# Kernel optimization log

Hardware: AMD Instinct MI355X
Metric: run time of the kernel (lower is better)

Reference implementation:

```python
import jax, jax.numpy as jnp
import numpy as np

D_MODEL = 1024
NUM_HEADS = 16
HEAD_DIM = D_MODEL // NUM_HEADS
ROT_DIM = 32
THETA = 10000.0
XPOS_SCALE_BASE = 512.0
GN_EPS = 1e-5


def setup_inputs() -> dict:
    key = jax.random.key(0)
    ks = jax.random.split(key, 12)
    d = D_MODEL
    s = 0.02
    return {
        "x": jax.random.normal(ks[0], (2, 2048, d), dtype=jnp.float32),
        "Wq": jax.random.normal(ks[1], (d, d), dtype=jnp.float32) * s,
        "bq": jnp.zeros((d,), jnp.float32),
        "Wk": jax.random.normal(ks[2], (d, d), dtype=jnp.float32) * s,
        "bk": jnp.zeros((d,), jnp.float32),
        "Wv": jax.random.normal(ks[3], (d, d), dtype=jnp.float32) * s,
        "bv": jnp.zeros((d,), jnp.float32),
        "Wg": jax.random.normal(ks[4], (d, d), dtype=jnp.float32) * s,
        "bg": jnp.zeros((d,), jnp.float32),
        "Wo": jax.random.normal(ks[5], (d, d), dtype=jnp.float32) * s,
        "bo": jnp.zeros((d,), jnp.float32),
        "gn_w": jnp.ones((NUM_HEADS,), jnp.float32),
        "gn_b": jnp.zeros((NUM_HEADS,), jnp.float32),
    }


def _rotate_half(x):
    # interleaved pair rotation: (x1, x2) -> (-x2, x1)
    x1 = x[..., 0::2]
    x2 = x[..., 1::2]
    return jnp.stack([-x2, x1], axis=-1).reshape(x.shape)


def _rotary_xpos(q, k):
    # q, k: [B, H, S, HEAD_DIM]; rotate first ROT_DIM dims with xpos scaling
    S = q.shape[-2]
    inv_freq = 1.0 / (THETA ** (jnp.arange(0, ROT_DIM, 2, dtype=jnp.float32) / ROT_DIM))
    t = jnp.arange(S, dtype=jnp.float32)
    freqs = jnp.repeat(t[:, None] * inv_freq[None, :], 2, axis=-1)  # [S, ROT_DIM]
    base = (jnp.arange(0, ROT_DIM, 2, dtype=jnp.float32) + 0.4 * ROT_DIM) / (1.4 * ROT_DIM)
    power = (t - S // 2) / XPOS_SCALE_BASE
    scale = jnp.repeat(base[None, :] ** power[:, None], 2, axis=-1)  # [S, ROT_DIM]
    cos, sin = jnp.cos(freqs), jnp.sin(freqs)

    def apply(x, s):
        xm, xr = x[..., :ROT_DIM], x[..., ROT_DIM:]
        xm = xm * (cos * s) + _rotate_half(xm) * (sin * s)
        return jnp.concatenate([xm, xr], axis=-1)

    return apply(q, scale), apply(k, 1.0 / scale)


def _decay_mask(S):
    # per-head causal decay mask, row-normalized by sqrt(row sum)
    h = jnp.arange(NUM_HEADS, dtype=jnp.float32)
    gamma = 1.0 - 2.0 ** (-5.0 - h)                       # [H]
    idx = jnp.arange(S)
    pw = (idx[:, None] - idx[None, :]).astype(jnp.float32)  # [S, S]
    mask = jnp.where(pw >= 0, gamma[:, None, None] ** pw, 0.0)  # [H, S, S]
    return mask / jnp.sqrt(jnp.sum(mask, axis=-1, keepdims=True))


def _heads(x):
    B, S, _ = x.shape
    return x.reshape(B, S, NUM_HEADS, HEAD_DIM).transpose(0, 2, 1, 3)


def reference(x, Wq, bq, Wk, bk, Wv, bv, Wg, bg, Wo, bo, gn_w, gn_b):
    B, S, d = x.shape
    q = _heads(x @ Wq + bq)
    k = _heads(x @ Wk + bk)
    v = _heads(x @ Wv + bv)
    q, k = _rotary_xpos(q, k)

    mask = _decay_mask(S)                                  # [H, S, S]
    scores = jnp.einsum("bhqd,bhkd->bhqk", q, k) * mask[None]
    ret = jnp.einsum("bhqk,bhkd->bhqd", scores, v)         # [B, H, S, HEAD_DIM]

    # GroupNorm(num_groups=H, num_channels=H): normalize each head over (S, D)
    mean = jnp.mean(ret, axis=(2, 3), keepdims=True)
    var = jnp.var(ret, axis=(2, 3), keepdims=True)
    ret = (ret - mean) / jnp.sqrt(var + GN_EPS)
    ret = ret * gn_w[None, :, None, None] + gn_b[None, :, None, None]

    concat = ret.transpose(0, 2, 1, 3).reshape(B, S, d)
    gate = jax.nn.silu(x @ Wg + bg)
    return (gate * concat) @ Wo + bo
```

## Files before the change

kernel.cpp:

```cpp
#include <hip/hip_runtime.h>
#include <math.h>

constexpr int B = 2;
constexpr int S = 2048;
constexpr int DMODEL = 1024;
constexpr int H = 16;
constexpr int M_TOT = B * S;
constexpr size_t MAT = (size_t)B * S * DMODEL;

typedef __attribute__((ext_vector_type(8))) __bf16 bf16x8;
typedef __attribute__((ext_vector_type(4))) float f32x4;

#define GLOAD16(g, l) __builtin_amdgcn_global_load_lds( \
    (const __attribute__((address_space(1))) void*)(g), \
    (__attribute__((address_space(3))) void*)(l), 16, 0, 0)

__device__ __forceinline__ float bf2f(__bf16 v) { return (float)v; }
__device__ __forceinline__ __bf16 f2bf(float v) { return (__bf16)v; }
__device__ __forceinline__ float silu(float z) { return z / (1.0f + expf(-z)); }

__global__ __launch_bounds__(256) void cvt_x_kernel(const float* __restrict__ x,
                                                    __bf16* __restrict__ xb)
{
    const size_t p = (size_t)blockIdx.x * 256 + threadIdx.x;
    const float4 a = reinterpret_cast<const float4*>(x)[2 * p];
    const float4 b = reinterpret_cast<const float4*>(x)[2 * p + 1];
    bf16x8 o;
    o[0] = f2bf(a.x); o[1] = f2bf(a.y); o[2] = f2bf(a.z); o[3] = f2bf(a.w);
    o[4] = f2bf(b.x); o[5] = f2bf(b.y); o[6] = f2bf(b.z); o[7] = f2bf(b.w);
    reinterpret_cast<bf16x8*>(xb)[p] = o;
}

__global__ __launch_bounds__(256) void transpose_w_kernel(
    const float* Wq, const float* Wk, const float* Wv, const float* Wg,
    const float* Wo, __bf16* __restrict__ wqkvg_t, __bf16* __restrict__ wo_t)
{
    __shared__ float tile[32][33];
    const int z = blockIdx.z;
    const float* W = (z == 0) ? Wq : (z == 1) ? Wk : (z == 2) ? Wv
                    : (z == 3) ? Wg : Wo;
    const int n0 = blockIdx.x * 32, k0 = blockIdx.y * 32;
    const int tx = threadIdx.x & 31, ty = threadIdx.x >> 5;

    #pragma unroll
    for (int i = 0; i < 32; i += 8)
        tile[ty + i][tx] = W[(size_t)(k0 + ty + i) * DMODEL + n0 + tx];
    __syncthreads();
    #pragma unroll
    for (int i = 0; i < 32; i += 8) {
        const int n = n0 + ty + i, kk = k0 + tx;
        const __bf16 val = f2bf(tile[tx][ty + i]);
        if (z < 4) wqkvg_t[((size_t)z * 1024 + n) * DMODEL + kk] = val;
        else       wo_t[(size_t)n * DMODEL + kk] = val;
    }
}

__global__ __launch_bounds__(256) void pack_bias_kernel(
    const float* bq, const float* bk, const float* bv, const float* bg,
    float* __restrict__ bqkvg)
{
    const int i = blockIdx.x * 256 + threadIdx.x;
    const float* src = ((i >> 10) == 0) ? bq : ((i >> 10) == 1) ? bk
                      : ((i >> 10) == 2) ? bv : bg;
    bqkvg[i] = src[i & 1023];
}

__device__ __forceinline__ bf16x8 ldsfrag(const char* base, int row, int kbyte)
{
    return *(const bf16x8*)(base + row * 64 + (kbyte ^ (((row >> 1) & 3) << 4)));
}

__device__ __forceinline__ void stage_panel(const __bf16* __restrict__ src,
                                            int srow0, int k0, char* bufbase,
                                            int tid, int wv)
{
    #pragma unroll
    for (int j = 0; j < 2; ++j) {
        const int r  = j * 128 + (tid >> 2);
        const int cb = ((tid & 3) * 16) ^ (((r >> 1) & 3) << 4);
        GLOAD16((const char*)(src + ((size_t)(srow0 + r) << 10) + k0) + cb,
                bufbase + j * 8192 + wv * 1024);
    }
}

__device__ __forceinline__ void stage_panel128(const __bf16* __restrict__ src,
                                               int srow0, int k0, char* bufbase,
                                               int tid, int wv)
{
    #pragma unroll
    for (int j = 0; j < 2; ++j) {
        const int r  = j * 64 + (tid >> 2);
        const int cb = ((tid & 3) * 16) ^ (((r >> 1) & 3) << 4);
        GLOAD16((const char*)(src + ((size_t)(srow0 + r) << 10) + k0) + cb,
                bufbase + j * 4096 + wv * 1024);
    }
}

__global__ __launch_bounds__(512) void gemm_qkvg_8ph(
    const __bf16* __restrict__ A, const __bf16* __restrict__ Bt,
    const float* __restrict__ bias,
    __bf16* o0, __bf16* o1, __bf16* o2, __bf16* o3)
{
    extern __shared__ char lds[];
    constexpr int NTK = 32;

    const int tid = threadIdx.x, wv = tid >> 6, ln = tid & 63;
    const int wm = wv >> 2, wn = wv & 3;

    int bid = blockIdx.x;
    bid = (bid & 7) * 32 + (bid >> 3);
    const int bx = bid & 15, by = bid >> 4;
    const int row0 = by * 256, col0 = bx * 256;

    const int lrow = ln & 15;
    const int kb   = (ln >> 4) * 16;

    f32x4 acc[8][4] = {};

    #pragma unroll
    for (int tt = 0; tt < 3; ++tt) {
        stage_panel(A,  row0, tt * 32, lds + tt * 16384, tid, wv);
        stage_panel(Bt, col0, tt * 32, lds + 65536 + tt * 16384, tid, wv);
    }
    asm volatile("s_waitcnt vmcnt(8)" ::: "memory");
    __builtin_amdgcn_s_barrier();
    __builtin_amdgcn_sched_barrier(0);

    for (int t = 0; t < NTK; ++t) {
        const char* ab = lds + (t & 3) * 16384;
        const char* bb = lds + 65536 + (t & 3) * 16384;
        bf16x8 af[8], bf[4];
        #pragma unroll
        for (int mf = 0; mf < 8; ++mf)
            af[mf] = ldsfrag(ab, wm * 128 + mf * 16 + lrow, kb);
        #pragma unroll
        for (int nf = 0; nf < 4; ++nf)
            bf[nf] = ldsfrag(bb, wn * 64 + nf * 16 + lrow, kb);

        if (t + 3 < NTK) {
            stage_panel(A,  row0, (t + 3) * 32,
                        lds + ((t + 3) & 3) * 16384, tid, wv);
            stage_panel(Bt, col0, (t + 3) * 32,
                        lds + 65536 + ((t + 3) & 3) * 16384, tid, wv);
        }

        __builtin_amdgcn_s_setprio(1);
        #pragma unroll
        for (int mf = 0; mf < 8; ++mf)
            #pragma unroll
            for (int nf = 0; nf < 4; ++nf)
                acc[mf][nf] = __builtin_amdgcn_mfma_f32_16x16x32_bf16(
                    af[mf], bf[nf], acc[mf][nf], 0, 0, 0);
        __builtin_amdgcn_s_setprio(0);

        if (t <= NTK - 4)
            asm volatile("s_waitcnt vmcnt(8)" ::: "memory");
        else if (t == NTK - 3)
            asm volatile("s_waitcnt vmcnt(4)" ::: "memory");
        else if (t == NTK - 2)
            asm volatile("s_waitcnt vmcnt(0)" ::: "memory");
        __builtin_amdgcn_s_barrier();
        __builtin_amdgcn_sched_barrier(0);
    }

    const int sel = col0 >> 10;
    __bf16* outp = (sel == 0) ? o0 : (sel == 1) ? o1 : (sel == 2) ? o2 : o3;
    const int cb0 = col0 & 1023;
    #pragma unroll
    for (int mf = 0; mf < 8; ++mf) {
        #pragma unroll
        for (int nf = 0; nf < 4; ++nf) {
            const int cl = cb0 + wn * 64 + nf * 16 + (ln & 15);
            const float bs = bias[col0 + wn * 64 + nf * 16 + (ln & 15)];
            #pragma unroll
            for (int reg = 0; reg < 4; ++reg) {
                const int r = row0 + wm * 128 + mf * 16 + (ln >> 4) * 4 + reg;
                outp[(size_t)r * 1024 + cl] = f2bf(acc[mf][nf][reg] + bs);
            }
        }
    }
}

__global__ __launch_bounds__(256) void gemm_wo_kernel(
    const __bf16* __restrict__ A, const __bf16* __restrict__ Bt,
    const float* __restrict__ bias, float* __restrict__ fout)
{
    __shared__ char lds[65536];
    constexpr int NTK = 32;

    const int tid = threadIdx.x, wv = tid >> 6, ln = tid & 63;
    const int row0 = blockIdx.y * 128, col0 = blockIdx.x * 128;
    const int wr = (wv >> 1) * 64, wc = (wv & 1) * 64;
    const int lrow = ln & 15, kb = (ln >> 4) * 16;

    f32x4 acc[4][4] = {};

    #pragma unroll
    for (int tt = 0; tt < 3; ++tt) {
        stage_panel128(A,  row0, tt * 32, lds + tt * 8192, tid, wv);
        stage_panel128(Bt, col0, tt * 32, lds + 32768 + tt * 8192, tid, wv);
    }
    asm volatile("s_waitcnt vmcnt(8)" ::: "memory");
    __builtin_amdgcn_s_barrier();
    __builtin_amdgcn_sched_barrier(0);

    for (int t = 0; t < NTK; ++t) {
        const char* ab = lds + (t & 3) * 8192;
        const char* bb = lds + 32768 + (t & 3) * 8192;
        bf16x8 af[4], bf[4];
        #pragma unroll
        for (int mi = 0; mi < 4; ++mi)
            af[mi] = ldsfrag(ab, wr + mi * 16 + lrow, kb);
        #pragma unroll
        for (int ni = 0; ni < 4; ++ni)
            bf[ni] = ldsfrag(bb, wc + ni * 16 + lrow, kb);

        if (t + 3 < NTK) {
            stage_panel128(A,  row0, (t + 3) * 32,
                           lds + ((t + 3) & 3) * 8192, tid, wv);
            stage_panel128(Bt, col0, (t + 3) * 32,
                           lds + 32768 + ((t + 3) & 3) * 8192, tid, wv);
        }

        __builtin_amdgcn_s_setprio(1);
        #pragma unroll
        for (int mi = 0; mi < 4; ++mi)
            #pragma unroll
            for (int ni = 0; ni < 4; ++ni)
                acc[mi][ni] = __builtin_amdgcn_mfma_f32_16x16x32_bf16(
                    af[mi], bf[ni], acc[mi][ni], 0, 0, 0);
        __builtin_amdgcn_s_setprio(0);

        if (t <= NTK - 4)
            asm volatile("s_waitcnt vmcnt(8)" ::: "memory");
        else if (t == NTK - 3)
            asm volatile("s_waitcnt vmcnt(4)" ::: "memory");
        else if (t == NTK - 2)
            asm volatile("s_waitcnt vmcnt(0)" ::: "memory");
        __builtin_amdgcn_s_barrier();
        __builtin_amdgcn_sched_barrier(0);
    }

    #pragma unroll
    for (int mi = 0; mi < 4; ++mi) {
        #pragma unroll
        for (int ni = 0; ni < 4; ++ni) {
            const int c = col0 + wc + ni * 16 + (ln & 15);
            const float bs = bias[c];
            #pragma unroll
            for (int reg = 0; reg < 4; ++reg) {
                const int r = row0 + wr + mi * 16 + (ln >> 4) * 4 + reg;
                fout[(size_t)r * DMODEL + c] = acc[mi][ni][reg] + bs;
            }
        }
    }
}

__global__ __launch_bounds__(256) void rotary_bf16_kernel(__bf16* __restrict__ q,
                                                          __bf16* __restrict__ k)
{
    const int bs = blockIdx.x;
    const int s  = bs & (S - 1);
    const int h  = threadIdx.x >> 4;
    const int j  = threadIdx.x & 15;
    const int sloc = s & 63;

    const float gamma = 1.0f - exp2f(-5.0f - (float)h);
    const float l2g   = log2f(gamma);
    const float wq = exp2f((float)(sloc + 1) * l2g);
    const float wk = exp2f((float)(63 - sloc) * l2g);

    const float inv_freq = powf(10000.0f, -(float)j / 16.0f);
    const float freq = (float)s * inv_freq;
    const float c  = cosf(freq);
    const float sn = sinf(freq);
    const float base = (2.0f * j + 0.4f * 32.0f) / (1.4f * 32.0f);
    const float p    = ((float)s - (float)(S / 2)) / 512.0f;
    const float sc   = powf(base, p);

    const size_t off = (size_t)bs * DMODEL + h * 64 + 2 * j;

    const float q0 = bf2f(q[off]), q1 = bf2f(q[off + 1]);
    q[off]     = f2bf((q0 * c - q1 * sn) * sc * wq);
    q[off + 1] = f2bf((q1 * c + q0 * sn) * sc * wq);

    const float isc = 1.0f / sc;
    const float k0 = bf2f(k[off]), k1 = bf2f(k[off + 1]);
    k[off]     = f2bf((k0 * c - k1 * sn) * isc * wk);
    k[off + 1] = f2bf((k1 * c + k0 * sn) * isc * wk);

    const size_t off2 = off + 32;
    q[off2]     = f2bf(bf2f(q[off2])     * wq);
    q[off2 + 1] = f2bf(bf2f(q[off2 + 1]) * wq);
    k[off2]     = f2bf(bf2f(k[off2])     * wk);
    k[off2 + 1] = f2bf(bf2f(k[off2 + 1]) * wk);
}

__global__ __launch_bounds__(256) void transpose_kv_kernel(
    const __bf16* __restrict__ kb, const __bf16* __restrict__ vb,
    __bf16* __restrict__ kt, __bf16* __restrict__ vt)
{
    __shared__ __bf16 tile[64][72];
    const int stile = blockIdx.x;
    const int h = blockIdx.y;
    const int b = blockIdx.z >> 1, which = blockIdx.z & 1;
    const __bf16* src = which ? kb : vb;
    __bf16* dst = which ? kt : vt;
    const int t = threadIdx.x;
    #pragma unroll
    for (int p = 0; p < 2; ++p) {
        const int ci = p * 256 + t;
        const int r = ci >> 3, c8 = (ci & 7) * 8;
        *reinterpret_cast<bf16x8*>(&tile[r][c8]) =
            *reinterpret_cast<const bf16x8*>(
                &src[(size_t)(b * S + stile * 64 + r) * DMODEL + h * 64 + c8]);
    }
    __syncthreads();
    #pragma unroll
    for (int p = 0; p < 2; ++p) {
        const int ci = p * 256 + t;
        const int d = ci >> 3, s8 = (ci & 7) * 8;
        bf16x8 o;
        #pragma unroll
        for (int w = 0; w < 8; ++w) o[w] = tile[s8 + w][d];
        *reinterpret_cast<bf16x8*>(
            &dst[((size_t)(b * 16 + h) * 64 + d) * 2048 + stile * 64 + s8]) = o;
    }
}

__global__ __launch_bounds__(256) void chunk_outer_kernel(
    const __bf16* __restrict__ kt, const __bf16* __restrict__ vt,
    float* __restrict__ U)
{
    __shared__ __bf16 kl[64 * 64];
    __shared__ __bf16 vl[64 * 64];
    const int c = blockIdx.x, h = blockIdx.y, b = blockIdx.z;
    const int bh = b * 16 + h;
    const size_t baset = (size_t)bh * 64 * 2048 + c * 64;
    const int t = threadIdx.x, wv = t >> 6, ln = t & 63;
    const int lrow = ln & 15, lk8 = (ln >> 4) * 8;

    #pragma unroll
    for (int p = 0; p < 2; ++p) {
        const int ci = p * 256 + t;
        const int r = ci >> 3, c8 = (ci & 7) * 8;
        const int off = r * 128 + ((c8 * 2) ^ ((r & 7) << 4));
        *(bf16x8*)((char*)kl + off) =
            *reinterpret_cast<const bf16x8*>(&kt[baset + (size_t)r * 2048 + c8]);
        *(bf16x8*)((char*)vl + off) =
            *reinterpret_cast<const bf16x8*>(&vt[baset + (size_t)r * 2048 + c8]);
    }
    __syncthreads();

    f32x4 uacc[4] = {};
    #pragma unroll
    for (int ks = 0; ks < 2; ++ks) {
        const int arow = wv * 16 + lrow;
        const bf16x8 af = *(const bf16x8*)((char*)vl + arow * 128 +
            (((ks * 32 + lk8) * 2) ^ ((arow & 7) << 4)));
        #pragma unroll
        for (int nf = 0; nf < 4; ++nf) {
            const int brow = nf * 16 + lrow;
            const bf16x8 bf_ = *(const bf16x8*)((char*)kl + brow * 128 +
                (((ks * 32 + lk8) * 2) ^ ((brow & 7) << 4)));
            uacc[nf] = __builtin_amdgcn_mfma_f32_16x16x32_bf16(
                af, bf_, uacc[nf], 0, 0, 0);
        }
    }

    const size_t ub = ((size_t)bh * 32 + c) * 4096;
    #pragma unroll
    for (int nf = 0; nf < 4; ++nf) {
        const int dk = nf * 16 + (ln & 15);
        #pragma unroll
        for (int reg = 0; reg < 4; ++reg) {
            const int dv = wv * 16 + (ln >> 4) * 4 + reg;
            U[ub + dv * 64 + dk] = uacc[nf][reg];
        }
    }
}

__global__ __launch_bounds__(256) void chunk_scan_kernel(
    const float* __restrict__ U, __bf16* __restrict__ St)
{
    const int dvq = blockIdx.x, bh = blockIdx.y;
    const int h = bh & 15;
    const float gamma = 1.0f - exp2f(-5.0f - (float)h);
    const float g64 = exp2f(64.0f * log2f(gamma));
    const int t = threadIdx.x;
    const int dk = t & 63;
    const int dv0 = dvq * 16 + (t >> 6) * 4;
    float s0 = 0.f, s1 = 0.f, s2 = 0.f, s3 = 0.f;
    const size_t ub = (size_t)bh * 32 * 4096;
    for (int c = 0; c < 32; ++c) {
        const size_t sb = ub + (size_t)c * 4096;
        St[sb + (dv0 + 0) * 64 + dk] = f2bf(s0);
        St[sb + (dv0 + 1) * 64 + dk] = f2bf(s1);
        St[sb + (dv0 + 2) * 64 + dk] = f2bf(s2);
        St[sb + (dv0 + 3) * 64 + dk] = f2bf(s3);
        s0 = g64 * s0 + U[sb + (dv0 + 0) * 64 + dk];
        s1 = g64 * s1 + U[sb + (dv0 + 1) * 64 + dk];
        s2 = g64 * s2 + U[sb + (dv0 + 2) * 64 + dk];
        s3 = g64 * s3 + U[sb + (dv0 + 3) * 64 + dk];
    }
}

__global__ __launch_bounds__(256) void retention_chunk_kernel(
    const __bf16* __restrict__ qg, const __bf16* __restrict__ kg,
    const __bf16* __restrict__ vt, const __bf16* __restrict__ St,
    float* __restrict__ ret)
{
    __shared__ __bf16 qh[64 * 64];
    __shared__ __bf16 kh[64 * 64];
    __shared__ __bf16 vl[64 * 64];
    __shared__ __bf16 sl[64 * 64];
    __shared__ __bf16 pl[64 * 64];

    const int c = blockIdx.x, h = blockIdx.y, b = blockIdx.z;
    const int bh = b * 16 + h;
    const int t = threadIdx.x, wv = t >> 6, ln = t & 63;
    const int lrow = ln & 15, lk8 = (ln >> 4) * 8;

    const float gamma = 1.0f - exp2f(-5.0f - (float)h);
    const float l2g   = log2f(gamma);
    const float gm64i = exp2f(-64.0f * l2g);
    const size_t rowbase = ((size_t)b * S + c * 64) * DMODEL + h * 64;
    const size_t vtb = (size_t)bh * 64 * 2048 + c * 64;
    const size_t stb = ((size_t)bh * 32 + c) * 4096;

    #pragma unroll
    for (int p = 0; p < 2; ++p) {
        const int ci = p * 256 + t;
        const int r = ci >> 3, c8 = (ci & 7) * 8;
        const int off = r * 128 + ((c8 * 2) ^ ((r & 7) << 4));
        *(bf16x8*)((char*)qh + off) =
            *reinterpret_cast<const bf16x8*>(&qg[rowbase + (size_t)r * DMODEL + c8]);
        *(bf16x8*)((char*)kh + off) =
            *reinterpret_cast<const bf16x8*>(&kg[rowbase + (size_t)r * DMODEL + c8]);
        *(bf16x8*)((char*)vl + off) =
            *reinterpret_cast<const bf16x8*>(&vt[vtb + (size_t)r * 2048 + c8]);
        *(bf16x8*)((char*)sl + off) =
            *reinterpret_cast<const bf16x8*>(&St[stb + r * 64 + c8]);
    }
    __syncthreads();

    f32x4 sacc[4] = {};
    #pragma unroll
    for (int ks = 0; ks < 2; ++ks) {
        const int qrow = wv * 16 + lrow;
        const bf16x8 qf = *(const bf16x8*)((char*)qh + qrow * 128 +
            (((ks * 32 + lk8) * 2) ^ ((qrow & 7) << 4)));
        #pragma unroll
        for (int mi = 0; mi < 4; ++mi) {
            const int krow = mi * 16 + lrow;
            const bf16x8 kf = *(const bf16x8*)((char*)kh + krow * 128 +
                (((ks * 32 + lk8) * 2) ^ ((krow & 7) << 4)));
            sacc[mi] = __builtin_amdgcn_mfma_f32_16x16x32_bf16(
                kf, qf, sacc[mi], 0, 0, 0);
        }
    }

    const int iw = wv * 16 + (ln & 15);
    #pragma unroll
    for (int mi = 0; mi < 4; ++mi) {
        ushort4 pk;
        unsigned short* pkp = (unsigned short*)&pk;
        #pragma unroll
        for (int reg = 0; reg < 4; ++reg) {
            const int j = mi * 16 + (ln >> 4) * 4 + reg;
            const float pv = (j <= iw) ? sacc[mi][reg] * gm64i : 0.0f;
            const __bf16 pb = f2bf(pv);
            pkp[reg] = *(const unsigned short*)&pb;
        }
        const int jb8 = mi * 16 + (ln >> 4) * 4;
        *(ushort4*)((char*)pl + iw * 128 + ((jb8 * 2) ^ ((iw & 7) << 4))) = pk;
    }

    f32x4 acc[4] = {};
    #pragma unroll
    for (int ks = 0; ks < 2; ++ks) {
        const int prow = wv * 16 + lrow;
        const bf16x8 pf = *(const bf16x8*)((char*)pl + prow * 128 +
            (((ks * 32 + lk8) * 2) ^ ((prow & 7) << 4)));
        const bf16x8 qf2 = *(const bf16x8*)((char*)qh + prow * 128 +
            (((ks * 32 + lk8) * 2) ^ ((prow & 7) << 4)));
        #pragma unroll
        for (int nd = 0; nd < 4; ++nd) {
            const int vrow = nd * 16 + lrow;
            const bf16x8 vf = *(const bf16x8*)((char*)vl + vrow * 128 +
                (((ks * 32 + lk8) * 2) ^ ((vrow & 7) << 4)));
            const bf16x8 sf = *(const bf16x8*)((char*)sl + vrow * 128 +
                (((ks * 32 + lk8) * 2) ^ ((vrow & 7) << 4)));
            acc[nd] = __builtin_amdgcn_mfma_f32_16x16x32_bf16(
                pf, vf, acc[nd], 0, 0, 0);
            acc[nd] = __builtin_amdgcn_mfma_f32_16x16x32_bf16(
                qf2, sf, acc[nd], 0, 0, 0);
        }
    }

    const float sc5h = exp2f(5.0f + (float)h);
    #pragma unroll
    for (int reg = 0; reg < 4; ++reg) {
        const int i = c * 64 + wv * 16 + (ln >> 4) * 4 + reg;
        const float omg = 1.0f - exp2f((float)(i + 1) * l2g);
        const float invn = rsqrtf(omg * sc5h);
        #pragma unroll
        for (int nd = 0; nd < 4; ++nd)
            ret[((size_t)b * S + i) * DMODEL + h * 64 + nd * 16 + (ln & 15)] =
                acc[nd][reg] * invn;
    }
}

__global__ __launch_bounds__(256) void gn_stats1_kernel(
    const float* __restrict__ ret, float* __restrict__ part)
{
    const int sl = blockIdx.x;
    const int bh = blockIdx.y;
    const int b = bh >> 4, h = bh & 15;
    const size_t rowbase = ((size_t)b * S + sl * 128) * DMODEL + h * 64;
    float sum = 0.0f, sq = 0.0f;
    #pragma unroll
    for (int it = 0; it < 8; ++it) {
        const int idx = it * 256 + threadIdx.x;
        const int row = idx >> 4;
        const int c4 = (idx & 15) * 4;
        const float4 v = *reinterpret_cast<const float4*>(
            &ret[rowbase + (size_t)row * DMODEL + c4]);
        sum += v.x + v.y + v.z + v.w;
        sq  += v.x * v.x + v.y * v.y + v.z * v.z + v.w * v.w;
    }
    #pragma unroll
    for (int o = 32; o > 0; o >>= 1) {
        sum += __shfl_down(sum, o, 64);
        sq  += __shfl_down(sq, o, 64);
    }
    __shared__ float rs[4], rq[4];
    const int wid = threadIdx.x >> 6, lane = threadIdx.x & 63;
    if (lane == 0) { rs[wid] = sum; rq[wid] = sq; }
    __syncthreads();
    if (threadIdx.x == 0) {
        part[(bh * 16 + sl) * 2 + 0] = rs[0] + rs[1] + rs[2] + rs[3];
        part[(bh * 16 + sl) * 2 + 1] = rq[0] + rq[1] + rq[2] + rq[3];
    }
}

__global__ __launch_bounds__(64) void gn_stats2_kernel(const float* __restrict__ part,
                                                       float* __restrict__ stats)
{
    const int bh = threadIdx.x;
    if (bh < 32) {
        float s = 0.0f, q2 = 0.0f;
        for (int i = 0; i < 16; ++i) {
            s  += part[(bh * 16 + i) * 2 + 0];
            q2 += part[(bh * 16 + i) * 2 + 1];
        }
        const float inv_n = 1.0f / (float)(S * 64);
        const float mean = s * inv_n;
        const float var  = q2 * inv_n - mean * mean;
        stats[bh * 2 + 0] = mean;
        stats[bh * 2 + 1] = rsqrtf(var + 1e-5f);
    }
}

__global__ __launch_bounds__(256) void gn_apply_kernel(
    const float* __restrict__ ret, const __bf16* __restrict__ g,
    __bf16* __restrict__ y, const float* __restrict__ stats,
    const float* __restrict__ gnw, const float* __restrict__ gnb)
{
    const size_t p = (size_t)blockIdx.x * 256 + threadIdx.x;
    const size_t el = p * 8;
    const int col = (int)(el & (DMODEL - 1));
    const int h   = col >> 6;
    const int b   = (int)(el >> 21);
    const int bh  = b * H + h;
    const float mean = stats[bh * 2 + 0];
    const float w    = stats[bh * 2 + 1] * gnw[h];
    const float bb   = gnb[h];

    const float4 r0 = reinterpret_cast<const float4*>(ret)[2 * p];
    const float4 r1 = reinterpret_cast<const float4*>(ret)[2 * p + 1];
    const bf16x8 gv = reinterpret_cast<const bf16x8*>(g)[p];
    bf16x8 o;
    o[0] = f2bf(((r0.x - mean) * w + bb) * silu(bf2f(gv[0])));
    o[1] = f2bf(((r0.y - mean) * w + bb) * silu(bf2f(gv[1])));
    o[2] = f2bf(((r0.z - mean) * w + bb) * silu(bf2f(gv[2])));
    o[3] = f2bf(((r0.w - mean) * w + bb) * silu(bf2f(gv[3])));
    o[4] = f2bf(((r1.x - mean) * w + bb) * silu(bf2f(gv[4])));
    o[5] = f2bf(((r1.y - mean) * w + bb) * silu(bf2f(gv[5])));
    o[6] = f2bf(((r1.z - mean) * w + bb) * silu(bf2f(gv[6])));
    o[7] = f2bf(((r1.w - mean) * w + bb) * silu(bf2f(gv[7])));
    reinterpret_cast<bf16x8*>(y)[p] = o;
}

extern "C" void kernel_launch(void* const* d_in, const int* in_sizes, int n_in,
                              void* d_out, int out_size, void* d_ws, size_t ws_size,
                              hipStream_t stream)
{
    const float* x   = (const float*)d_in[0];
    const float* Wq  = (const float*)d_in[1];
    const float* bq  = (const float*)d_in[2];
    const float* Wk  = (const float*)d_in[3];
    const float* bk  = (const float*)d_in[4];
    const float* Wv  = (const float*)d_in[5];
    const float* bv  = (const float*)d_in[6];
    const float* Wg  = (const float*)d_in[7];
    const float* bg  = (const float*)d_in[8];
    const float* Wo  = (const float*)d_in[9];
    const float* bo  = (const float*)d_in[10];
    const float* gnw = (const float*)d_in[11];
    const float* gnb = (const float*)d_in[12];
    float* out = (float*)d_out;

    char* w = (char*)d_ws;
    __bf16* xb      = (__bf16*)w;               w += MAT * 2;
    __bf16* wqkvg_t = (__bf16*)w;               w += MAT * 2;
    __bf16* wo_t    = (__bf16*)w;               w += (size_t)DMODEL * DMODEL * 2;
    float*  bqkvg   = (float*)w;                w += 4096 * 4;
    __bf16* qb      = (__bf16*)w;               w += MAT * 2;
    __bf16* kb      = (__bf16*)w;               w += MAT * 2;
    __bf16* vb      = (__bf16*)w;               w += MAT * 2;
    __bf16* gb      = (__bf16*)w;               w += MAT * 2;
    float*  ret     = (float*)w;                w += MAT * 4;
    __bf16* yb      = (__bf16*)w;               w += MAT * 2;
    float*  part    = (float*)w;                w += 512 * 2 * 4;
    float*  stats   = (float*)w;                w += 64 * 4;
    __bf16* vt = xb;
    __bf16* kt = yb;
    float*  U  = ret;
    __bf16* St = (__bf16*)wqkvg_t;

    static_cast<void>(hipFuncSetAttribute(
        reinterpret_cast<const void*>(gemm_qkvg_8ph),
        hipFuncAttributeMaxDynamicSharedMemorySize, 131072));

    cvt_x_kernel<<<2048, 256, 0, stream>>>(x, xb);
    {
        dim3 grid(32, 32, 5);
        transpose_w_kernel<<<grid, 256, 0, stream>>>(Wq, Wk, Wv, Wg, Wo,
                                                     wqkvg_t, wo_t);
    }
    pack_bias_kernel<<<16, 256, 0, stream>>>(bq, bk, bv, bg, bqkvg);

    gemm_qkvg_8ph<<<256, 512, 131072, stream>>>(
        xb, wqkvg_t, bqkvg, qb, kb, vb, gb);

    rotary_bf16_kernel<<<B * S, 256, 0, stream>>>(qb, kb);
    {
        dim3 grid(32, 16, 4);
        transpose_kv_kernel<<<grid, 256, 0, stream>>>(kb, vb, kt, vt);
    }

    {
        dim3 grid(32, 16, 2);
        chunk_outer_kernel<<<grid, 256, 0, stream>>>(kt, vt, U);
    }
    {
        dim3 grid(4, 32);
        chunk_scan_kernel<<<grid, 256, 0, stream>>>(U, St);
    }
    {
        dim3 grid(32, 16, 2);
        retention_chunk_kernel<<<grid, 256, 0, stream>>>(qb, kb, vt, St, ret);
    }

    {
        dim3 grid(16, 32);
        gn_stats1_kernel<<<grid, 256, 0, stream>>>(ret, part);
    }
    gn_stats2_kernel<<<1, 64, 0, stream>>>(part, stats);
    gn_apply_kernel<<<2048, 256, 0, stream>>>(ret, gb, yb, stats, gnw, gnb);

    {
        dim3 grid(8, 32);
        gemm_wo_kernel<<<grid, 256, 0, stream>>>(yb, wo_t, bo, out);
    }
}
```

Baseline: 126.6 us.

## Retile QKVG GEMM, vectorize rotary, fuse transpose and GN stats into neighbors

The QKVG projection GEMM moves from 256x256 tiles with a 4-stage, 128KB dynamic-LDS pipeline to 256x128 tiles with static 48KB double buffering, giving 512 blocks and more blocks per CU. The rotary kernel is rewritten to process 8 contiguous bf16 elements per thread with vector loads and stores. The K/V transpose is fused into the chunk outer-product kernel, and the GroupNorm partial sums are computed inside the retention kernel, which removes two launches and a full re-read of the fp32 ret buffer. In exchange the GEMM's prefetch depth drops from three stages to one, which may expose more global-load latency.

New measurement: 130.4 us. 3.0% more time.

```diff
diff --git a/kernel.cpp b/kernel.cpp
--- a/kernel.cpp
+++ b/kernel.cpp
@@ -70,19 +70,6 @@
     return *(const bf16x8*)(base + row * 64 + (kbyte ^ (((row >> 1) & 3) << 4)));
 }
 
-__device__ __forceinline__ void stage_panel(const __bf16* __restrict__ src,
-                                            int srow0, int k0, char* bufbase,
-                                            int tid, int wv)
-{
-    #pragma unroll
-    for (int j = 0; j < 2; ++j) {
-        const int r  = j * 128 + (tid >> 2);
-        const int cb = ((tid & 3) * 16) ^ (((r >> 1) & 3) << 4);
-        GLOAD16((const char*)(src + ((size_t)(srow0 + r) << 10) + k0) + cb,
-                bufbase + j * 8192 + wv * 1024);
-    }
-}
-
 __device__ __forceinline__ void stage_panel128(const __bf16* __restrict__ src,
                                                int srow0, int k0, char* bufbase,
                                                int tid, int wv)
@@ -96,61 +83,147 @@
     }
 }
 
-__global__ __launch_bounds__(512) void gemm_qkvg_8ph(
+__global__ __launch_bounds__(512, 4) void gemm_qkvg(
     const __bf16* __restrict__ A, const __bf16* __restrict__ Bt,
     const float* __restrict__ bias,
     __bf16* o0, __bf16* o1, __bf16* o2, __bf16* o3)
 {
-    extern __shared__ char lds[];
+    __shared__ char lds[49152];
     constexpr int NTK = 32;
 
     const int tid = threadIdx.x, wv = tid >> 6, ln = tid & 63;
-    const int wm = wv >> 2, wn = wv & 3;
+    const int wm = wv >> 1, wn = wv & 1;
 
     int bid = blockIdx.x;
-    bid = (bid & 7) * 32 + (bid >> 3);
-    const int bx = bid & 15, by = bid >> 4;
-    const int row0 = by * 256, col0 = bx * 256;
+    bid = (bid & 7) * 64 + (bid >> 3);
+    const int bx = bid & 31, by = bid >> 5;
+    const int row0 = by * 256, col0 = bx * 128;
 
     const int lrow = ln & 15;
     const int kb   = (ln >> 4) * 16;
 
-    f32x4 acc[8][4] = {};
-
-    #pragma unroll
-    for (int tt = 0; tt < 3; ++tt) {
-        stage_panel(A,  row0, tt * 32, lds + tt * 16384, tid, wv);
-        stage_panel(Bt, col0, tt * 32, lds + 65536 + tt * 16384, tid, wv);
-    }
-    asm volatile("s_waitcnt vmcnt(8)" ::: "memory");
-    __builtin_amdgcn_s_barrier();
-    __builtin_amdgcn_sched_barrier(0);
+    f32x4 acc[4][4] = {};
+
+    auto stageA = [&](int k0, char* buf) {
+        #pragma unroll
+        for (int j = 0; j < 2; ++j) {
+            const int r  = j * 128 + (tid >> 2);
+            const int cb = ((tid & 3) * 16) ^ (((r >> 1) & 3) << 4);
+            GLOAD16((const char*)(A + ((size_t)(row0 + r) << 10) + k0) + cb,
+                    buf + j * 8192 + wv * 1024);
+        }
+    };
+    auto stageB = [&](int k0, char* buf) {
+        const int r  = tid >> 2;
+        const int cb = ((tid & 3) * 16) ^ (((r >> 1) & 3) << 4);
+        GLOAD16((const char*)(Bt + ((size_t)(col0 + r) << 10) + k0) + cb,
+                buf + wv * 1024);
+    };
+
+    stageA(0, lds);
+    stageB(0, lds + 32768);
 
     for (int t = 0; t < NTK; ++t) {
-        const char* ab = lds + (t & 3) * 16384;
-        const char* bb = lds + 65536 + (t & 3) * 16384;
-        bf16x8 af[8], bf[4];
-        #pragma unroll
-        for (int mf = 0; mf < 8; ++mf)
-            af[mf] = ldsfrag(ab, wm * 128 + mf * 16 + lrow, kb);
+        char* ab = lds + (t & 1) * 16384;
+        char* bb = lds + 32768 + (t & 1) * 8192;
+
+        if (t + 1 < NTK) {
+            stageA((t + 1) * 32, lds + ((t + 1) & 1) * 16384);
+            stageB((t + 1) * 32, lds + 32768 + ((t + 1) & 1) * 8192);
+            asm volatile("s_waitcnt vmcnt(3)" ::: "memory");
+        } else {
+            asm volatile("s_waitcnt vmcnt(0)" ::: "memory");
+        }
+        __builtin_amdgcn_s_barrier();
+        __builtin_amdgcn_sched_barrier(0);
+
+        bf16x8 af[4], bf[4];
+        #pragma unroll
+        for (int mf = 0; mf < 4; ++mf)
+            af[mf] = ldsfrag(ab, wm * 64 + mf * 16 + lrow, kb);
         #pragma unroll
         for (int nf = 0; nf < 4; ++nf)
             bf[nf] = ldsfrag(bb, wn * 64 + nf * 16 + lrow, kb);
 
-        if (t + 3 < NTK) {
-            stage_panel(A,  row0, (t + 3) * 32,
-                        lds + ((t + 3) & 3) * 16384, tid, wv);
-            stage_panel(Bt, col0, (t + 3) * 32,
-                        lds + 65536 + ((t + 3) & 3) * 16384, tid, wv);
-        }
-
         __builtin_amdgcn_s_setprio(1);
         #pragma unroll
-        for (int mf = 0; mf < 8; ++mf)
+        for (int mf = 0; mf < 4; ++mf)
             #pragma unroll
             for (int nf = 0; nf < 4; ++nf)
                 acc[mf][nf] = __builtin_amdgcn_mfma_f32_16x16x32_bf16(
                     af[mf], bf[nf], acc[mf][nf], 0, 0, 0);
+        __builtin_amdgcn_s_setprio(0);
+
+        __builtin_amdgcn_s_barrier();
+        __builtin_amdgcn_sched_barrier(0);
+    }
+
+    const int sel = col0 >> 10;
+    __bf16* outp = (sel == 0) ? o0 : (sel == 1) ? o1 : (sel == 2) ? o2 : o3;
+    const int cb0 = col0 & 1023;
+    #pragma unroll
+    for (int mf = 0; mf < 4; ++mf) {
+        #pragma unroll
+        for (int nf = 0; nf < 4; ++nf) {
+            const int cl = cb0 + wn * 64 + nf * 16 + (ln & 15);
+            const float bs = bias[col0 + wn * 64 + nf * 16 + (ln & 15)];
+            #pragma unroll
+            for (int reg = 0; reg < 4; ++reg) {
+                const int r = row0 + wm * 64 + mf * 16 + (ln >> 4) * 4 + reg;
+                outp[(size_t)r * 1024 + cl] = f2bf(acc[mf][nf][reg] + bs);
+            }
+        }
+    }
+}
+
+__global__ __launch_bounds__(256) void gemm_wo_kernel(
+    const __bf16* __restrict__ A, const __bf16* __restrict__ Bt,
+    const float* __restrict__ bias, float* __restrict__ fout)
+{
+    __shared__ char lds[65536];
+    constexpr int NTK = 32;
+
+    const int tid = threadIdx.x, wv = tid >> 6, ln = tid & 63;
+    const int row0 = blockIdx.y * 128, col0 = blockIdx.x * 128;
+    const int wr = (wv >> 1) * 64, wc = (wv & 1) * 64;
+    const int lrow = ln & 15, kb = (ln >> 4) * 16;
+
+    f32x4 acc[4][4] = {};
+
+    #pragma unroll
+    for (int tt = 0; tt < 3; ++tt) {
+        stage_panel128(A,  row0, tt * 32, lds + tt * 8192, tid, wv);
+        stage_panel128(Bt, col0, tt * 32, lds + 32768 + tt * 8192, tid, wv);
+    }
+    asm volatile("s_waitcnt vmcnt(8)" ::: "memory");
+    __builtin_amdgcn_s_barrier();
+    __builtin_amdgcn_sched_barrier(0);
+
+    for (int t = 0; t < NTK; ++t) {
+        const char* ab = lds + (t & 3) * 8192;
+        const char* bb = lds + 32768 + (t & 3) * 8192;
+        bf16x8 af[4], bf[4];
+        #pragma unroll
+        for (int mi = 0; mi < 4; ++mi)
+            af[mi] = ldsfrag(ab, wr + mi * 16 + lrow, kb);
+        #pragma unroll
+        for (int ni = 0; ni < 4; ++ni)
+            bf[ni] = ldsfrag(bb, wc + ni * 16 + lrow, kb);
+
+        if (t + 3 < NTK) {
+            stage_panel128(A,  row0, (t + 3) * 32,
+                           lds + ((t + 3) & 3) * 8192, tid, wv);
+            stage_panel128(Bt, col0, (t + 3) * 32,
+                           lds + 32768 + ((t + 3) & 3) * 8192, tid, wv);
+        }
+
+        __builtin_amdgcn_s_setprio(1);
+        #pragma unroll
+        for (int mi = 0; mi < 4; ++mi)
+            #pragma unroll
+            for (int ni = 0; ni < 4; ++ni)
+                acc[mi][ni] = __builtin_amdgcn_mfma_f32_16x16x32_bf16(
+                    af[mi], bf[ni], acc[mi][ni], 0, 0, 0);
         __builtin_amdgcn_s_setprio(0);
 
         if (t <= NTK - 4)
@@ -163,84 +236,6 @@
         __builtin_amdgcn_sched_barrier(0);
     }
 
-    const int sel = col0 >> 10;
-    __bf16* outp = (sel == 0) ? o0 : (sel == 1) ? o1 : (sel == 2) ? o2 : o3;
-    const int cb0 = col0 & 1023;
-    #pragma unroll
-    for (int mf = 0; mf < 8; ++mf) {
-        #pragma unroll
-        for (int nf = 0; nf < 4; ++nf) {
-            const int cl = cb0 + wn * 64 + nf * 16 + (ln & 15);
-            const float bs = bias[col0 + wn * 64 + nf * 16 + (ln & 15)];
-            #pragma unroll
-            for (int reg = 0; reg < 4; ++reg) {
-                const int r = row0 + wm * 128 + mf * 16 + (ln >> 4) * 4 + reg;
-                outp[(size_t)r * 1024 + cl] = f2bf(acc[mf][nf][reg] + bs);
-            }
-        }
-    }
-}
-
-__global__ __launch_bounds__(256) void gemm_wo_kernel(
-    const __bf16* __restrict__ A, const __bf16* __restrict__ Bt,
-    const float* __restrict__ bias, float* __restrict__ fout)
-{
-    __shared__ char lds[65536];
-    constexpr int NTK = 32;
-
-    const int tid = threadIdx.x, wv = tid >> 6, ln = tid & 63;
-    const int row0 = blockIdx.y * 128, col0 = blockIdx.x * 128;
-    const int wr = (wv >> 1) * 64, wc = (wv & 1) * 64;
-    const int lrow = ln & 15, kb = (ln >> 4) * 16;
-
-    f32x4 acc[4][4] = {};
-
-    #pragma unroll
-    for (int tt = 0; tt < 3; ++tt) {
-        stage_panel128(A,  row0, tt * 32, lds + tt * 8192, tid, wv);
-        stage_panel128(Bt, col0, tt * 32, lds + 32768 + tt * 8192, tid, wv);
-    }
-    asm volatile("s_waitcnt vmcnt(8)" ::: "memory");
-    __builtin_amdgcn_s_barrier();
-    __builtin_amdgcn_sched_barrier(0);
-
-    for (int t = 0; t < NTK; ++t) {
-        const char* ab = lds + (t & 3) * 8192;
-        const char* bb = lds + 32768 + (t & 3) * 8192;
-        bf16x8 af[4], bf[4];
-        #pragma unroll
-        for (int mi = 0; mi < 4; ++mi)
-            af[mi] = ldsfrag(ab, wr + mi * 16 + lrow, kb);
-        #pragma unroll
-        for (int ni = 0; ni < 4; ++ni)
-            bf[ni] = ldsfrag(bb, wc + ni * 16 + lrow, kb);
-
-        if (t + 3 < NTK) {
-            stage_panel128(A,  row0, (t + 3) * 32,
-                           lds + ((t + 3) & 3) * 8192, tid, wv);
-            stage_panel128(Bt, col0, (t + 3) * 32,
-                           lds + 32768 + ((t + 3) & 3) * 8192, tid, wv);
-        }
-
-        __builtin_amdgcn_s_setprio(1);
-        #pragma unroll
-        for (int mi = 0; mi < 4; ++mi)
-            #pragma unroll
-            for (int ni = 0; ni < 4; ++ni)
-                acc[mi][ni] = __builtin_amdgcn_mfma_f32_16x16x32_bf16(
-                    af[mi], bf[ni], acc[mi][ni], 0, 0, 0);
-        __builtin_amdgcn_s_setprio(0);
-
-        if (t <= NTK - 4)
-            asm volatile("s_waitcnt vmcnt(8)" ::: "memory");
-        else if (t == NTK - 3)
-            asm volatile("s_waitcnt vmcnt(4)" ::: "memory");
-        else if (t == NTK - 2)
-            asm volatile("s_waitcnt vmcnt(0)" ::: "memory");
-        __builtin_amdgcn_s_barrier();
-        __builtin_amdgcn_sched_barrier(0);
-    }
-
     #pragma unroll
     for (int mi = 0; mi < 4; ++mi) {
         #pragma unroll
@@ -259,10 +254,12 @@
 __global__ __launch_bounds__(256) void rotary_bf16_kernel(__bf16* __restrict__ q,
                                                           __bf16* __restrict__ k)
 {
-    const int bs = blockIdx.x;
-    const int s  = bs & (S - 1);
-    const int h  = threadIdx.x >> 4;
-    const int j  = threadIdx.x & 15;
+    const size_t p = (size_t)blockIdx.x * 256 + threadIdx.x;
+    const size_t el = p * 8;
+    const int bs = (int)(el >> 10);
+    const int col = (int)(el & 1023);
+    const int h = col >> 6, d0 = col & 63;
+    const int s = bs & (S - 1);
     const int sloc = s & 63;
 
     const float gamma = 1.0f - exp2f(-5.0f - (float)h);
@@ -270,85 +267,82 @@
     const float wq = exp2f((float)(sloc + 1) * l2g);
     const float wk = exp2f((float)(63 - sloc) * l2g);
 
-    const float inv_freq = powf(10000.0f, -(float)j / 16.0f);
-    const float freq = (float)s * inv_freq;
-    const float c  = cosf(freq);
-    const float sn = sinf(freq);
-    const float base = (2.0f * j + 0.4f * 32.0f) / (1.4f * 32.0f);
-    const float p    = ((float)s - (float)(S / 2)) / 512.0f;
-    const float sc   = powf(base, p);
-
-    const size_t off = (size_t)bs * DMODEL + h * 64 + 2 * j;
-
-    const float q0 = bf2f(q[off]), q1 = bf2f(q[off + 1]);
-    q[off]     = f2bf((q0 * c - q1 * sn) * sc * wq);
-    q[off + 1] = f2bf((q1 * c + q0 * sn) * sc * wq);
-
-    const float isc = 1.0f / sc;
-    const float k0 = bf2f(k[off]), k1 = bf2f(k[off + 1]);
-    k[off]     = f2bf((k0 * c - k1 * sn) * isc * wk);
-    k[off + 1] = f2bf((k1 * c + k0 * sn) * isc * wk);
-
-    const size_t off2 = off + 32;
-    q[off2]     = f2bf(bf2f(q[off2])     * wq);
-    q[off2 + 1] = f2bf(bf2f(q[off2 + 1]) * wq);
-    k[off2]     = f2bf(bf2f(k[off2])     * wk);
-    k[off2 + 1] = f2bf(bf2f(k[off2 + 1]) * wk);
-}
-
-__global__ __launch_bounds__(256) void transpose_kv_kernel(
-    const __bf16* __restrict__ kb, const __bf16* __restrict__ vb,
-    __bf16* __restrict__ kt, __bf16* __restrict__ vt)
-{
-    __shared__ __bf16 tile[64][72];
-    const int stile = blockIdx.x;
-    const int h = blockIdx.y;
-    const int b = blockIdx.z >> 1, which = blockIdx.z & 1;
-    const __bf16* src = which ? kb : vb;
-    __bf16* dst = which ? kt : vt;
-    const int t = threadIdx.x;
+    bf16x8 qv = reinterpret_cast<const bf16x8*>(q)[p];
+    bf16x8 kv = reinterpret_cast<const bf16x8*>(k)[p];
+    bf16x8 qo, ko;
+
+    if (d0 < 32) {
+        const float pexp = ((float)s - (float)(S / 2)) / 512.0f;
+        #pragma unroll
+        for (int w = 0; w < 4; ++w) {
+            const int j = (d0 >> 1) + w;
+            const float inv_freq = powf(10000.0f, -(float)j / 16.0f);
+            const float freq = (float)s * inv_freq;
+            const float c  = cosf(freq);
+            const float sn = sinf(freq);
+            const float base = (2.0f * j + 0.4f * 32.0f) / (1.4f * 32.0f);
+            const float sc   = powf(base, pexp);
+
+            const float q0 = bf2f(qv[2 * w]), q1 = bf2f(qv[2 * w + 1]);
+            qo[2 * w]     = f2bf((q0 * c - q1 * sn) * sc * wq);
+            qo[2 * w + 1] = f2bf((q1 * c + q0 * sn) * sc * wq);
+            const float isc = 1.0f / sc;
+            const float k0 = bf2f(kv[2 * w]), k1 = bf2f(kv[2 * w + 1]);
+            ko[2 * w]     = f2bf((k0 * c - k1 * sn) * isc * wk);
+            ko[2 * w + 1] = f2bf((k1 * c + k0 * sn) * isc * wk);
+        }
+    } else {
+        #pragma unroll
+        for (int w = 0; w < 8; ++w) {
+            qo[w] = f2bf(bf2f(qv[w]) * wq);
+            ko[w] = f2bf(bf2f(kv[w]) * wk);
+        }
+    }
+    reinterpret_cast<bf16x8*>(q)[p] = qo;
+    reinterpret_cast<bf16x8*>(k)[p] = ko;
+}
+
+__global__ __launch_bounds__(256) void chunk_prep_kernel(
+    const __bf16* __restrict__ kg, const __bf16* __restrict__ vg,
+    __bf16* __restrict__ vt, float* __restrict__ U)
+{
+    __shared__ __bf16 ktile[64][72];
+    __shared__ __bf16 vtile[64][72];
+    __shared__ __bf16 ktl[64 * 64];
+    __shared__ __bf16 vtl[64 * 64];
+
+    const int c = blockIdx.x, h = blockIdx.y, b = blockIdx.z;
+    const int bh = b * 16 + h;
+    const int t = threadIdx.x, wv = t >> 6, ln = t & 63;
+    const int lrow = ln & 15, lk8 = (ln >> 4) * 8;
+    const size_t rowbase = ((size_t)b * S + c * 64) * DMODEL + h * 64;
+
     #pragma unroll
     for (int p = 0; p < 2; ++p) {
         const int ci = p * 256 + t;
         const int r = ci >> 3, c8 = (ci & 7) * 8;
-        *reinterpret_cast<bf16x8*>(&tile[r][c8]) =
-            *reinterpret_cast<const bf16x8*>(
-                &src[(size_t)(b * S + stile * 64 + r) * DMODEL + h * 64 + c8]);
+        *reinterpret_cast<bf16x8*>(&ktile[r][c8]) =
+            *reinterpret_cast<const bf16x8*>(&kg[rowbase + (size_t)r * DMODEL + c8]);
+        *reinterpret_cast<bf16x8*>(&vtile[r][c8]) =
+            *reinterpret_cast<const bf16x8*>(&vg[rowbase + (size_t)r * DMODEL + c8]);
     }
     __syncthreads();
+
     #pragma unroll
     for (int p = 0; p < 2; ++p) {
         const int ci = p * 256 + t;
         const int d = ci >> 3, s8 = (ci & 7) * 8;
-        bf16x8 o;
-        #pragma unroll
-        for (int w = 0; w < 8; ++w) o[w] = tile[s8 + w][d];
+        bf16x8 ok, ov;
+        #pragma unroll
+        for (int w = 0; w < 8; ++w) {
+            ok[w] = ktile[s8 + w][d];
+            ov[w] = vtile[s8 + w][d];
+        }
         *reinterpret_cast<bf16x8*>(
-            &dst[((size_t)(b * 16 + h) * 64 + d) * 2048 + stile * 64 + s8]) = o;
-    }
-}
-
-__global__ __launch_bounds__(256) void chunk_outer_kernel(
-    const __bf16* __restrict__ kt, const __bf16* __restrict__ vt,
-    float* __restrict__ U)
-{
-    __shared__ __bf16 kl[64 * 64];
-    __shared__ __bf16 vl[64 * 64];
-    const int c = blockIdx.x, h = blockIdx.y, b = blockIdx.z;
-    const int bh = b * 16 + h;
-    const size_t baset = (size_t)bh * 64 * 2048 + c * 64;
-    const int t = threadIdx.x, wv = t >> 6, ln = t & 63;
-    const int lrow = ln & 15, lk8 = (ln >> 4) * 8;
-
-    #pragma unroll
-    for (int p = 0; p < 2; ++p) {
-        const int ci = p * 256 + t;
-        const int r = ci >> 3, c8 = (ci & 7) * 8;
-        const int off = r * 128 + ((c8 * 2) ^ ((r & 7) << 4));
-        *(bf16x8*)((char*)kl + off) =
-            *reinterpret_cast<const bf16x8*>(&kt[baset + (size_t)r * 2048 + c8]);
-        *(bf16x8*)((char*)vl + off) =
-            *reinterpret_cast<const bf16x8*>(&vt[baset + (size_t)r * 2048 + c8]);
+            &vt[((size_t)bh * 64 + d) * 2048 + c * 64 + s8]) = ov;
+        const int off = d * 128 + ((s8 * 2) ^ ((d & 7) << 4));
+        *(bf16x8*)((char*)ktl + off) = ok;
+        *(bf16x8*)((char*)vtl + off) = ov;
     }
     __syncthreads();
 
@@ -356,12 +350,12 @@
     #pragma unroll
     for (int ks = 0; ks < 2; ++ks) {
         const int arow = wv * 16 + lrow;
-        const bf16x8 af = *(const bf16x8*)((char*)vl + arow * 128 +
+        const bf16x8 af = *(const bf16x8*)((char*)vtl + arow * 128 +
             (((ks * 32 + lk8) * 2) ^ ((arow & 7) << 4)));
         #pragma unroll
         for (int nf = 0; nf < 4; ++nf) {
             const int brow = nf * 16 + lrow;
-            const bf16x8 bf_ = *(const bf16x8*)((char*)kl + brow * 128 +
+            const bf16x8 bf_ = *(const bf16x8*)((char*)ktl + brow * 128 +
                 (((ks * 32 + lk8) * 2) ^ ((brow & 7) << 4)));
             uacc[nf] = __builtin_amdgcn_mfma_f32_16x16x32_bf16(
                 af, bf_, uacc[nf], 0, 0, 0);
@@ -408,13 +402,14 @@
 __global__ __launch_bounds__(256) void retention_chunk_kernel(
     const __bf16* __restrict__ qg, const __bf16* __restrict__ kg,
     const __bf16* __restrict__ vt, const __bf16* __restrict__ St,
-    float* __restrict__ ret)
+    float* __restrict__ ret, float* __restrict__ part)
 {
     __shared__ __bf16 qh[64 * 64];
     __shared__ __bf16 kh[64 * 64];
     __shared__ __bf16 vl[64 * 64];
     __shared__ __bf16 sl[64 * 64];
     __shared__ __bf16 pl[64 * 64];
+    __shared__ float rs[4], rq[4];
 
     const int c = blockIdx.x, h = blockIdx.y, b = blockIdx.z;
     const int bh = b * 16 + h;
@@ -499,48 +494,30 @@
     }
 
     const float sc5h = exp2f(5.0f + (float)h);
+    float psum = 0.0f, psq = 0.0f;
     #pragma unroll
     for (int reg = 0; reg < 4; ++reg) {
         const int i = c * 64 + wv * 16 + (ln >> 4) * 4 + reg;
         const float omg = 1.0f - exp2f((float)(i + 1) * l2g);
         const float invn = rsqrtf(omg * sc5h);
         #pragma unroll
-        for (int nd = 0; nd < 4; ++nd)
-            ret[((size_t)b * S + i) * DMODEL + h * 64 + nd * 16 + (ln & 15)] =
-                acc[nd][reg] * invn;
-    }
-}
-
-__global__ __launch_bounds__(256) void gn_stats1_kernel(
-    const float* __restrict__ ret, float* __restrict__ part)
-{
-    const int sl = blockIdx.x;
-    const int bh = blockIdx.y;
-    const int b = bh >> 4, h = bh & 15;
-    const size_t rowbase = ((size_t)b * S + sl * 128) * DMODEL + h * 64;
-    float sum = 0.0f, sq = 0.0f;
-    #pragma unroll
-    for (int it = 0; it < 8; ++it) {
-        const int idx = it * 256 + threadIdx.x;
-        const int row = idx >> 4;
-        const int c4 = (idx & 15) * 4;
-        const float4 v = *reinterpret_cast<const float4*>(
-            &ret[rowbase + (size_t)row * DMODEL + c4]);
-        sum += v.x + v.y + v.z + v.w;
-        sq  += v.x * v.x + v.y * v.y + v.z * v.z + v.w * v.w;
+        for (int nd = 0; nd < 4; ++nd) {
+            const float v = acc[nd][reg] * invn;
+            ret[((size_t)b * S + i) * DMODEL + h * 64 + nd * 16 + (ln & 15)] = v;
+            psum += v;
+            psq  += v * v;
+        }
     }
     #pragma unroll
     for (int o = 32; o > 0; o >>= 1) {
-        sum += __shfl_down(sum, o, 64);
-        sq  += __shfl_down(sq, o, 64);
-    }
-    __shared__ float rs[4], rq[4];
-    const int wid = threadIdx.x >> 6, lane = threadIdx.x & 63;
-    if (lane == 0) { rs[wid] = sum; rq[wid] = sq; }
+        psum += __shfl_down(psum, o, 64);
+        psq  += __shfl_down(psq, o, 64);
+    }
+    if (ln == 0) { rs[wv] = psum; rq[wv] = psq; }
     __syncthreads();
-    if (threadIdx.x == 0) {
-        part[(bh * 16 + sl) * 2 + 0] = rs[0] + rs[1] + rs[2] + rs[3];
-        part[(bh * 16 + sl) * 2 + 1] = rq[0] + rq[1] + rq[2] + rq[3];
+    if (t == 0) {
+        part[((size_t)bh * 32 + c) * 2 + 0] = rs[0] + rs[1] + rs[2] + rs[3];
+        part[((size_t)bh * 32 + c) * 2 + 1] = rq[0] + rq[1] + rq[2] + rq[3];
     }
 }
 
@@ -550,9 +527,9 @@
     const int bh = threadIdx.x;
     if (bh < 32) {
         float s = 0.0f, q2 = 0.0f;
-        for (int i = 0; i < 16; ++i) {
-            s  += part[(bh * 16 + i) * 2 + 0];
-            q2 += part[(bh * 16 + i) * 2 + 1];
+        for (int i = 0; i < 32; ++i) {
+            s  += part[(bh * 32 + i) * 2 + 0];
+            q2 += part[(bh * 32 + i) * 2 + 1];
         }
         const float inv_n = 1.0f / (float)(S * 64);
         const float mean = s * inv_n;
@@ -622,16 +599,11 @@
     __bf16* gb      = (__bf16*)w;               w += MAT * 2;
     float*  ret     = (float*)w;                w += MAT * 4;
     __bf16* yb      = (__bf16*)w;               w += MAT * 2;
-    float*  part    = (float*)w;                w += 512 * 2 * 4;
+    float*  part    = (float*)w;                w += 2048 * 4;
     float*  stats   = (float*)w;                w += 64 * 4;
     __bf16* vt = xb;
-    __bf16* kt = yb;
     float*  U  = ret;
     __bf16* St = (__bf16*)wqkvg_t;
-
-    static_cast<void>(hipFuncSetAttribute(
-        reinterpret_cast<const void*>(gemm_qkvg_8ph),
-        hipFuncAttributeMaxDynamicSharedMemorySize, 131072));
 
     cvt_x_kernel<<<2048, 256, 0, stream>>>(x, xb);
     {
@@ -641,18 +613,13 @@
     }
     pack_bias_kernel<<<16, 256, 0, stream>>>(bq, bk, bv, bg, bqkvg);
 
-    gemm_qkvg_8ph<<<256, 512, 131072, stream>>>(
-        xb, wqkvg_t, bqkvg, qb, kb, vb, gb);
-
-    rotary_bf16_kernel<<<B * S, 256, 0, stream>>>(qb, kb);
-    {
-        dim3 grid(32, 16, 4);
-        transpose_kv_kernel<<<grid, 256, 0, stream>>>(kb, vb, kt, vt);
-    }
+    gemm_qkvg<<<512, 512, 0, stream>>>(xb, wqkvg_t, bqkvg, qb, kb, vb, gb);
+
+    rotary_bf16_kernel<<<2048, 256, 0, stream>>>(qb, kb);
 
     {
         dim3 grid(32, 16, 2);
-        chunk_outer_kernel<<<grid, 256, 0, stream>>>(kt, vt, U);
+        chunk_prep_kernel<<<grid, 256, 0, stream>>>(kb, vb, vt, U);
     }
     {
         dim3 grid(4, 32);
@@ -660,13 +627,10 @@
     }
     {
         dim3 grid(32, 16, 2);
-        retention_chunk_kernel<<<grid, 256, 0, stream>>>(qb, kb, vt, St, ret);
-    }
-
-    {
-        dim3 grid(16, 32);
-        gn_stats1_kernel<<<grid, 256, 0, stream>>>(ret, part);
-    }
+        retention_chunk_kernel<<<grid, 256, 0, stream>>>(qb, kb, vt, St,
+                                                         ret, part);
+    }
+
     gn_stats2_kernel<<<1, 64, 0, stream>>>(part, stats);
     gn_apply_kernel<<<2048, 256, 0, stream>>>(ret, gb, yb, stats, gnw, gnb);
 
```
